# Optimization experiments

Measured on AMD Instinct MI355X. Metric: run time of the kernel, lower is better.

## Reference

```python
import jax, jax.numpy as jnp
import numpy as np

RADIUS = 2
TOP_K = 5000
SCORES_TH = 0.2
TEMPERATURE = 0.1


def setup_inputs() -> dict:
    key = jax.random.key(0)
    score_map = jax.random.uniform(key, (16, 1, 1024, 1024), dtype=jnp.float32)
    return {"score_map": score_map}


def _simple_nms(s, kernel_size):
    # max_pool2d(kernel, stride=1, pad=kernel//2) then keep only local maxima
    pad = kernel_size // 2
    mp = jax.lax.reduce_window(
        s, -jnp.inf, jax.lax.max,
        window_dimensions=(1, 1, kernel_size, kernel_size),
        window_strides=(1, 1, 1, 1),
        padding=((0, 0), (0, 0), (pad, pad), (pad, pad)))
    return jnp.where(s == mp, s, jnp.zeros_like(s))


def reference(score_map):
    B, _, H, W = score_map.shape
    ksize = 2 * RADIUS + 1

    # --- NMS (applied twice, as in the torch code) ---
    nms = score_map
    for _ in range(2):
        nms = _simple_nms(nms, ksize)

    # --- top-k + threshold ---
    flat = nms.reshape(B, -1)                      # (B, H*W)
    k = min(TOP_K, flat.shape[1])
    topk_scores, topk_idx = jax.lax.top_k(flat, k)  # sorted desc -> valid set is a prefix
    valid = topk_scores > SCORES_TH                 # (B, K)
    y_pix = topk_idx // W                           # (B, K) int
    x_pix = topk_idx % W

    # --- batched windowed soft-argmax refinement (boundary-aware) ---
    half = RADIUS
    d = jnp.arange(-half, half + 1)                 # (ksize,)
    dy = d[:, None] * jnp.ones((1, ksize), d.dtype) # (ksize, ksize)
    dx = d[None, :] * jnp.ones((ksize, 1), d.dtype)
    yy = y_pix[:, :, None, None] + dy               # (B, K, ksize, ksize)
    xx = x_pix[:, :, None, None] + dx
    inb = (yy >= 0) & (yy < H) & (xx >= 0) & (xx < W)
    yy_c = jnp.clip(yy, 0, H - 1)
    xx_c = jnp.clip(xx, 0, W - 1)

    sm = score_map[:, 0]                            # (B, H, W)
    b_idx = jnp.arange(B)[:, None, None, None]
    patch = sm[b_idx, yy_c, xx_c]                   # (B, K, ksize, ksize)

    # softmax over valid window entries only (out-of-bounds masked to -1e9,
    # equivalent to the torch code slicing away boundary pixels)
    logits = jnp.where(inb, patch / TEMPERATURE, jnp.float32(-1e9))
    wts = jax.nn.softmax(logits.reshape(B, k, -1), axis=-1)  # (B, K, ksize*ksize)

    dxf = dx.reshape(-1).astype(score_map.dtype)
    dyf = dy.reshape(-1).astype(score_map.dtype)
    off_x = jnp.einsum('bkw,w->bk', wts, dxf)
    off_y = jnp.einsum('bkw,w->bk', wts, dyf)

    kpts = jnp.stack([x_pix.astype(score_map.dtype) + off_x,
                      y_pix.astype(score_map.dtype) + off_y], axis=-1)  # (B, K, 2)

    # invalid (below-threshold) keypoints are zero-padded, matching the torch padding
    keypoints = jnp.where(valid[..., None], kpts, jnp.zeros_like(kpts))
    scores = jnp.where(valid, topk_scores, jnp.zeros_like(topk_scores))
    return keypoints, scores
```

## Files before the change

kernel.cpp:

```cpp
#include <hip/hip_runtime.h>
#include <math.h>

#define B 16
#define H 1024
#define W 1024
#define TOPK 5000
#define SCORES_TH 0.2f

#define CAP 65536
#define SELCAP 8192
#define NB2 9831
#define OFFB2 510361
#define GS2 9840
#define SCHUNK 10
#define CSTRIDE 32

#define XSTRIPS 9
#define YSTRIPS 64
#define SROWS 16
#define SCOLS 124
#define WCAP 224

__global__ __launch_bounds__(256) void nms_wave(
    const float* __restrict__ s,
    unsigned* __restrict__ counts,
    unsigned long long* __restrict__ cand)
{
    __shared__ unsigned long long wbuf[4][WCAP];
    __shared__ unsigned wcnt[4];

    const int tid  = threadIdx.x;
    const int w    = tid >> 6;
    const int lane = tid & 63;
    const int gw   = blockIdx.x * 4 + w;
    const int xs   = gw % XSTRIPS;
    const int t    = gw / XSTRIPS;
    const int ys   = t & 63;
    const int b    = t >> 6;

    if (lane == 0) wcnt[w] = 0;

    const float* sb = s + (size_t)b * (H * W);
    const int c0 = xs * SCOLS - 2 + 2 * lane;
    const int y0 = ys * SROWS;
    const bool in0  = (c0 >= 0) & (c0 < W);
    const bool in1  = (c0 + 1 >= 0) & (c0 + 1 < W);
    const bool fast = in0 & in1;
    const bool emitlane = (lane >= 1) & (lane <= 62);

    float ha0 = -INFINITY, ha1 = -INFINITY, ha2 = -INFINITY, ha3 = -INFINITY;
    float hb0 = -INFINITY, hb1 = -INFINITY, hb2 = -INFINITY, hb3 = -INFINITY;
    float va1 = -INFINITY, va2 = -INFINITY;
    float vb1 = -INFINITY, vb2 = -INFINITY;

    #pragma unroll 4
    for (int gy = y0 - 2; gy <= y0 + SROWS + 1; ++gy) {
        float a, bq;
        const bool yin = (gy >= 0) & (gy < H);
        if (yin & fast) {
            float2 v = *(const float2*)(sb + (size_t)gy * W + c0);
            a = v.x; bq = v.y;
        } else {
            a  = (yin & in0) ? sb[(size_t)gy * W + c0]     : -INFINITY;
            bq = (yin & in1) ? sb[(size_t)gy * W + c0 + 1] : -INFINITY;
        }

        float p   = fmaxf(a, bq);
        float pm1 = __shfl_up(p, 1);
        float pp1 = __shfl_down(p, 1);
        float ap1 = __shfl_down(a, 1);
        float bm1 = __shfl_up(bq, 1);
        float hma = fmaxf(fmaxf(pm1, p), ap1);
        float hmb = fmaxf(fmaxf(bm1, p), pp1);

        if (gy >= y0 + 2) {
            float vma = fmaxf(fmaxf(fmaxf(ha0, ha1), fmaxf(ha2, ha3)), hma);
            float vmb = fmaxf(fmaxf(fmaxf(hb0, hb1), fmaxf(hb2, hb3)), hmb);
            bool pka = emitlane & in0 & (va2 > SCORES_TH) & (va2 == vma);
            bool pkb = emitlane & in1 & (vb2 > SCORES_TH) & (vb2 == vmb);
            if (pka | pkb) {
                int r = gy - 2;
                if (pka) {
                    unsigned idx = (unsigned)(r * W + c0);
                    unsigned long long key =
                        ((unsigned long long)__float_as_uint(va2) << 32) | (unsigned)(~idx);
                    unsigned pi = atomicAdd(&wcnt[w], 1u);
                    if (pi < WCAP) wbuf[w][pi] = key;
                    else {
                        unsigned gp = atomicAdd(&counts[b * CSTRIDE], 1u);
                        if (gp < CAP) cand[(size_t)b * CAP + gp] = key;
                    }
                }
                if (pkb) {
                    unsigned idx = (unsigned)(r * W + c0 + 1);
                    unsigned long long key =
                        ((unsigned long long)__float_as_uint(vb2) << 32) | (unsigned)(~idx);
                    unsigned pi = atomicAdd(&wcnt[w], 1u);
                    if (pi < WCAP) wbuf[w][pi] = key;
                    else {
                        unsigned gp = atomicAdd(&counts[b * CSTRIDE], 1u);
                        if (gp < CAP) cand[(size_t)b * CAP + gp] = key;
                    }
                }
            }
        }

        ha0 = ha1; ha1 = ha2; ha2 = ha3; ha3 = hma;
        hb0 = hb1; hb1 = hb2; hb2 = hb3; hb3 = hmb;
        va2 = va1; va1 = a;
        vb2 = vb1; vb1 = bq;
    }

    unsigned n = wcnt[w]; if (n > WCAP) n = WCAP;
    unsigned base = 0;
    if (lane == 0) base = atomicAdd(&counts[b * CSTRIDE], n);
    base = __shfl(base, 0);
    for (unsigned k = (unsigned)lane; k < n; k += 64)
        if (base + k < CAP) cand[(size_t)b * CAP + base + k] = wbuf[w][k];
}

__global__ __launch_bounds__(1024) void scan_scatter(
    const unsigned* __restrict__ counts,
    const unsigned long long* __restrict__ cand,
    unsigned* __restrict__ G,
    unsigned* __restrict__ selC,
    unsigned long long* __restrict__ sel)
{
    const int b = blockIdx.x;
    __shared__ unsigned I[NB2 + 1];
    __shared__ unsigned csum[1024];
    __shared__ int Tsh;
    const int tid = threadIdx.x;

    for (int i = tid; i < NB2 + 1; i += 1024) I[i] = 0;
    if (tid == 0) Tsh = 0;
    __syncthreads();

    unsigned M = counts[b * CSTRIDE]; if (M > CAP) M = CAP;
    const unsigned long long* cb = cand + (size_t)b * CAP;

    for (unsigned i = tid; i < M; i += 1024) {
        unsigned bits = (unsigned)(cb[i] >> 32);
        int bk = (int)(bits >> 11) - OFFB2;
        bk = bk < 0 ? 0 : (bk > NB2 - 1 ? NB2 - 1 : bk);
        atomicAdd(&I[bk], 1u);
    }
    __syncthreads();

    unsigned local = 0;
    #pragma unroll
    for (int u = 0; u < SCHUNK; ++u) {
        int r = tid * SCHUNK + u;
        if (r < NB2) local += I[NB2 - 1 - r];
    }
    csum[tid] = local;
    __syncthreads();
    for (int off = 1; off < 1024; off <<= 1) {
        unsigned v = (tid >= off) ? csum[tid - off] : 0u;
        __syncthreads();
        csum[tid] += v;
        __syncthreads();
    }
    unsigned run = (tid == 0) ? 0u : csum[tid - 1];
    #pragma unroll
    for (int u = 0; u < SCHUNK; ++u) {
        int r = tid * SCHUNK + u;
        if (r < NB2) {
            int bk = NB2 - 1 - r;
            run += I[bk];
            I[bk] = run;
        }
    }
    __syncthreads();

    int localT = -1;
    #pragma unroll
    for (int u = 0; u < SCHUNK; ++u) {
        int r = tid * SCHUNK + u;
        if (r < NB2) {
            int bk = NB2 - 1 - r;
            if (I[bk] >= TOPK && bk > localT) localT = bk;
        }
    }
    if (localT >= 0) atomicMax(&Tsh, localT);
    __syncthreads();
    const int T = Tsh;
    if (tid == 0) selC[b] = I[T];

    unsigned* Gb = G + (size_t)b * GS2;
    for (int i = tid; i < NB2 + 1; i += 1024) Gb[i] = I[i];
    __syncthreads();

    for (unsigned i = tid; i < M; i += 1024) {
        unsigned long long key = cb[i];
        unsigned bits = (unsigned)(key >> 32);
        int bk = (int)(bits >> 11) - OFFB2;
        bk = bk < 0 ? 0 : (bk > NB2 - 1 ? NB2 - 1 : bk);
        if (bk >= T) {
            unsigned p = atomicAdd(&I[bk + 1], 1u);
            if (p < SELCAP) sel[(size_t)b * SELCAP + p] = key;
        }
    }
}

__global__ __launch_bounds__(256) void rank_refine(
    const float* __restrict__ s,
    const unsigned long long* __restrict__ sel,
    const unsigned* __restrict__ selC,
    const unsigned* __restrict__ G,
    float* __restrict__ out)
{
    const int b = blockIdx.y;
    unsigned C = selC[b]; if (C > SELCAP) C = SELCAP;
    const int tid = threadIdx.x;
    const unsigned g = blockIdx.x * 64u + (unsigned)(tid >> 2);
    const int l = tid & 3;

    if (g >= C) {
        if (g < TOPK && l == 0) {
            out[((size_t)b * TOPK + g) * 2 + 0] = 0.0f;
            out[((size_t)b * TOPK + g) * 2 + 1] = 0.0f;
            out[(size_t)B * TOPK * 2 + (size_t)b * TOPK + g] = 0.0f;
        }
        return;
    }

    const unsigned long long* sb = sel + (size_t)b * SELCAP;
    const unsigned long long my = sb[g];
    unsigned bits = (unsigned)(my >> 32);
    int bk = (int)(bits >> 11) - OFFB2;
    bk = bk < 0 ? 0 : (bk > NB2 - 1 ? NB2 - 1 : bk);

    const unsigned* Gb = G + (size_t)b * GS2;
    unsigned start = Gb[bk + 1], end = Gb[bk];
    if (end > SELCAP) end = SELCAP;
    unsigned rank = 0;
    for (unsigned j = start + (unsigned)l; j < end; j += 4)
        rank += (sb[j] > my) ? 1u : 0u;

    float v = __uint_as_float(bits);
    unsigned idx = ~((unsigned)my);
    int y = (int)(idx >> 10), x = (int)(idx & 1023);
    const float* smb = s + (size_t)b * (H * W);
    float wsum = 0.f, ox = 0.f, oy = 0.f;
    for (int c = l; c < 25; c += 4) {
        int dy = c / 5 - 2, dx = c - (c / 5) * 5 - 2;
        int yy = y + dy, xx = x + dx;
        bool inb = (yy >= 0 && yy < H && xx >= 0 && xx < W);
        int yc = min(max(yy, 0), H - 1), xc = min(max(xx, 0), W - 1);
        float p = smb[yc * W + xc];
        float lg = inb ? p * 10.0f : -1e9f;
        float e = expf(lg);
        wsum += e; ox += e * (float)dx; oy += e * (float)dy;
    }
    rank += __shfl_xor(rank, 1); rank += __shfl_xor(rank, 2);
    wsum += __shfl_xor(wsum, 1); wsum += __shfl_xor(wsum, 2);
    ox   += __shfl_xor(ox, 1);   ox   += __shfl_xor(ox, 2);
    oy   += __shfl_xor(oy, 1);   oy   += __shfl_xor(oy, 2);

    unsigned frank = start + rank;
    if (l == 0 && frank < TOPK) {
        float offx = ox / wsum, offy = oy / wsum;
        out[((size_t)b * TOPK + frank) * 2 + 0] = (float)x + offx;
        out[((size_t)b * TOPK + frank) * 2 + 1] = (float)y + offy;
        out[(size_t)B * TOPK * 2 + (size_t)b * TOPK + frank] = v;
    }
}

extern "C" void kernel_launch(void* const* d_in, const int* in_sizes, int n_in,
                              void* d_out, int out_size, void* d_ws, size_t ws_size,
                              hipStream_t stream)
{
    const float* s = (const float*)d_in[0];
    float* out = (float*)d_out;
    char* ws = (char*)d_ws;

    size_t off = 0;
    unsigned* counts        = (unsigned*)(ws + off);  off += 2048;
    unsigned* selC          = (unsigned*)(ws + off);  off += 64;
    unsigned* G             = (unsigned*)(ws + off);  off += (size_t)B * GS2 * 4;
    unsigned long long* sel = (unsigned long long*)(ws + off); off += (size_t)B * SELCAP * 8;
    unsigned long long* cand= (unsigned long long*)(ws + off);

    hipMemsetAsync(counts, 0, 2048, stream);

    nms_wave<<<dim3(XSTRIPS * YSTRIPS * B / 4), dim3(256), 0, stream>>>(s, counts, cand);
    scan_scatter<<<dim3(B), dim3(1024), 0, stream>>>(counts, cand, G, selC, sel);
    rank_refine<<<dim3(SELCAP * 4 / 256, B), dim3(256), 0, stream>>>(s, sel, selC, G, out);
}
```

Before: 100.00 us.

## Widen NMS strips to four columns per lane with float4 loads

Each lane of the NMS wave now processes four adjacent columns instead of two, loading them with float4 reads. Strips become 252 columns wide (5 per row instead of 9), which cuts the 4-column halo overhead and the shuffle count per output pixel. In exchange each lane holds more ring-buffer registers, the grid has fewer waves, and strips at the image edges take the scalar load path.

After: 84.99 us. -15.0%, faster.

```diff
diff --git a/kernel.cpp b/kernel.cpp
--- a/kernel.cpp
+++ b/kernel.cpp
@@ -15,10 +15,10 @@
 #define SCHUNK 10
 #define CSTRIDE 32
 
-#define XSTRIPS 9
+#define XSTRIPS 5
 #define YSTRIPS 64
 #define SROWS 16
-#define SCOLS 124
+#define SCOLS 252
 #define WCAP 224
 
 __global__ __launch_bounds__(256) void nms_wave(
@@ -35,66 +35,71 @@
     const int gw   = blockIdx.x * 4 + w;
     const int xs   = gw % XSTRIPS;
     const int t    = gw / XSTRIPS;
-    const int ys   = t & 63;
+    const int ys   = t & (YSTRIPS - 1);
     const int b    = t >> 6;
 
     if (lane == 0) wcnt[w] = 0;
 
     const float* sb = s + (size_t)b * (H * W);
-    const int c0 = xs * SCOLS - 2 + 2 * lane;
+    const int c0 = xs * SCOLS - 2 + 4 * lane;
     const int y0 = ys * SROWS;
-    const bool in0  = (c0 >= 0) & (c0 < W);
-    const bool in1  = (c0 + 1 >= 0) & (c0 + 1 < W);
-    const bool fast = in0 & in1;
-    const bool emitlane = (lane >= 1) & (lane <= 62);
-
-    float ha0 = -INFINITY, ha1 = -INFINITY, ha2 = -INFINITY, ha3 = -INFINITY;
-    float hb0 = -INFINITY, hb1 = -INFINITY, hb2 = -INFINITY, hb3 = -INFINITY;
-    float va1 = -INFINITY, va2 = -INFINITY;
-    float vb1 = -INFINITY, vb2 = -INFINITY;
+    const bool wfast = (xs > 0) & (xs < XSTRIPS - 1);
+
+    bool inb[4], emitok[4];
+    #pragma unroll
+    for (int j = 0; j < 4; ++j) {
+        int col = c0 + j, idx4 = 4 * lane + j;
+        inb[j]    = (col >= 0) & (col < W);
+        emitok[j] = inb[j] & (idx4 >= 2) & (idx4 <= 253);
+    }
+
+    float ring[4][4], p1[4], p2[4];
+    #pragma unroll
+    for (int j = 0; j < 4; ++j) {
+        ring[j][0] = ring[j][1] = ring[j][2] = ring[j][3] = -INFINITY;
+        p1[j] = p2[j] = -INFINITY;
+    }
 
     #pragma unroll 4
     for (int gy = y0 - 2; gy <= y0 + SROWS + 1; ++gy) {
-        float a, bq;
+        float a[4];
         const bool yin = (gy >= 0) & (gy < H);
-        if (yin & fast) {
-            float2 v = *(const float2*)(sb + (size_t)gy * W + c0);
-            a = v.x; bq = v.y;
+        if (yin & wfast) {
+            float4 v = *(const float4*)(sb + (size_t)gy * W + c0);
+            a[0] = v.x; a[1] = v.y; a[2] = v.z; a[3] = v.w;
+        } else if (yin) {
+            #pragma unroll
+            for (int j = 0; j < 4; ++j)
+                a[j] = inb[j] ? sb[(size_t)gy * W + c0 + j] : -INFINITY;
         } else {
-            a  = (yin & in0) ? sb[(size_t)gy * W + c0]     : -INFINITY;
-            bq = (yin & in1) ? sb[(size_t)gy * W + c0 + 1] : -INFINITY;
-        }
-
-        float p   = fmaxf(a, bq);
-        float pm1 = __shfl_up(p, 1);
-        float pp1 = __shfl_down(p, 1);
-        float ap1 = __shfl_down(a, 1);
-        float bm1 = __shfl_up(bq, 1);
-        float hma = fmaxf(fmaxf(pm1, p), ap1);
-        float hmb = fmaxf(fmaxf(bm1, p), pp1);
+            #pragma unroll
+            for (int j = 0; j < 4; ++j) a[j] = -INFINITY;
+        }
+
+        float pm01 = fmaxf(a[0], a[1]);
+        float pm12 = fmaxf(a[1], a[2]);
+        float pm23 = fmaxf(a[2], a[3]);
+        float Lh  = __shfl_up(pm23, 1);
+        float La3 = __shfl_up(a[3], 1);
+        float Ra0 = __shfl_down(a[0], 1);
+        float Rp  = __shfl_down(pm01, 1);
+        float h[4];
+        h[0] = fmaxf(fmaxf(Lh,  pm01), a[2]);
+        h[1] = fmaxf(fmaxf(La3, pm01), pm23);
+        h[2] = fmaxf(fmaxf(pm01, pm23), Ra0);
+        h[3] = fmaxf(fmaxf(pm12, pm23), Rp);
 
         if (gy >= y0 + 2) {
-            float vma = fmaxf(fmaxf(fmaxf(ha0, ha1), fmaxf(ha2, ha3)), hma);
-            float vmb = fmaxf(fmaxf(fmaxf(hb0, hb1), fmaxf(hb2, hb3)), hmb);
-            bool pka = emitlane & in0 & (va2 > SCORES_TH) & (va2 == vma);
-            bool pkb = emitlane & in1 & (vb2 > SCORES_TH) & (vb2 == vmb);
-            if (pka | pkb) {
-                int r = gy - 2;
-                if (pka) {
-                    unsigned idx = (unsigned)(r * W + c0);
+            const int r = gy - 2;
+            #pragma unroll
+            for (int j = 0; j < 4; ++j) {
+                float vm = fmaxf(fmaxf(fmaxf(ring[j][0], ring[j][1]),
+                                       fmaxf(ring[j][2], ring[j][3])), h[j]);
+                bool pk = emitok[j] & (p2[j] > SCORES_TH) & (p2[j] == vm);
+                if (pk) {
+                    unsigned idx = (unsigned)(r * W + c0 + j);
                     unsigned long long key =
-                        ((unsigned long long)__float_as_uint(va2) << 32) | (unsigned)(~idx);
-                    unsigned pi = atomicAdd(&wcnt[w], 1u);
-                    if (pi < WCAP) wbuf[w][pi] = key;
-                    else {
-                        unsigned gp = atomicAdd(&counts[b * CSTRIDE], 1u);
-                        if (gp < CAP) cand[(size_t)b * CAP + gp] = key;
-                    }
-                }
-                if (pkb) {
-                    unsigned idx = (unsigned)(r * W + c0 + 1);
-                    unsigned long long key =
-                        ((unsigned long long)__float_as_uint(vb2) << 32) | (unsigned)(~idx);
+                        ((unsigned long long)__float_as_uint(p2[j]) << 32) | (unsigned)(~idx);
                     unsigned pi = atomicAdd(&wcnt[w], 1u);
                     if (pi < WCAP) wbuf[w][pi] = key;
                     else {
@@ -105,10 +110,12 @@
             }
         }
 
-        ha0 = ha1; ha1 = ha2; ha2 = ha3; ha3 = hma;
-        hb0 = hb1; hb1 = hb2; hb2 = hb3; hb3 = hmb;
-        va2 = va1; va1 = a;
-        vb2 = vb1; vb1 = bq;
+        #pragma unroll
+        for (int j = 0; j < 4; ++j) {
+            ring[j][0] = ring[j][1]; ring[j][1] = ring[j][2];
+            ring[j][2] = ring[j][3]; ring[j][3] = h[j];
+            p2[j] = p1[j]; p1[j] = a[j];
+        }
     }
 
     unsigned n = wcnt[w]; if (n > WCAP) n = WCAP;
```
